# Performance work log

Hardware: AMD Instinct MI355X
Metric: run time of the kernel (lower is better)

The kernel has to match this reference:

```python
import jax, jax.numpy as jnp
import numpy as np

WIN_SIZE = 11
WIN_SIGMA = 1.5
DATA_RANGE = 255.0
K1, K2 = 0.01, 0.03


def _gauss_win():
    # matches _fspecial_gauss_1d(11, 1.5)
    coords = jnp.arange(WIN_SIZE, dtype=jnp.float32) - WIN_SIZE // 2
    g = jnp.exp(-(coords ** 2) / (2.0 * WIN_SIGMA ** 2))
    return g / g.sum()


def _gaussian_filter(x, win):
    # separable depthwise blur, 'valid' padding (padding=0 in torch), groups=C
    C = x.shape[1]
    dn = ('NCHW', 'OIHW', 'NCHW')
    kh = jnp.tile(win.reshape(1, 1, WIN_SIZE, 1), (C, 1, 1, 1))
    kw = jnp.tile(win.reshape(1, 1, 1, WIN_SIZE), (C, 1, 1, 1))
    out = jax.lax.conv_general_dilated(x, kh, (1, 1), 'VALID',
                                       dimension_numbers=dn, feature_group_count=C)
    out = jax.lax.conv_general_dilated(out, kw, (1, 1), 'VALID',
                                       dimension_numbers=dn, feature_group_count=C)
    return out


def setup_inputs() -> dict:
    key = jax.random.key(0)
    k1, k2 = jax.random.split(key)
    shape = (16, 3, 512, 512)
    X = jax.random.uniform(k1, shape, dtype=jnp.float32) * DATA_RANGE
    Y = jax.random.uniform(k2, shape, dtype=jnp.float32) * DATA_RANGE
    return {'X': X, 'Y': Y}


def reference(X, Y):
    win = _gauss_win()
    C1 = (K1 * DATA_RANGE) ** 2
    C2 = (K2 * DATA_RANGE) ** 2
    mu1 = _gaussian_filter(X, win)
    mu2 = _gaussian_filter(Y, win)
    mu1_sq = mu1 * mu1
    mu2_sq = mu2 * mu2
    mu1_mu2 = mu1 * mu2
    sigma1_sq = _gaussian_filter(X * X, win) - mu1_sq
    sigma2_sq = _gaussian_filter(Y * Y, win) - mu2_sq
    sigma12 = _gaussian_filter(X * Y, win) - mu1_mu2
    cs_map = (2.0 * sigma12 + C2) / (sigma1_sq + sigma2_sq + C2)
    ssim_map = (2.0 * mu1_mu2 + C1) / (mu1_sq + mu2_sq + C1) * cs_map
    # torch: mean over channel dim then squeeze(0) (no-op for N>1)
    ssim_map = jnp.mean(ssim_map, axis=1)  # [N, H-10, W-10]
    return 1.0 - ssim_map
```

## Files before the change

kernel.cpp:

```cpp
#include <hip/hip_runtime.h>


namespace {

constexpr int NN = 16, CC = 3, HH = 512, WW = 512;
constexpr int OH = HH - 10, OW = WW - 10;
constexpr int TW = 64, TH = 32;
constexpr int SR = 48, SC = 80;
constexpr int PIT = 80;
constexpr int HPITCH = 56;
constexpr float C1c = 6.5025f;
constexpr float C2c = 58.5225f;

typedef _Float16 half8   __attribute__((ext_vector_type(8)));
typedef _Float16 half4   __attribute__((ext_vector_type(4)));
typedef float    floatv4 __attribute__((ext_vector_type(4)));

__device__ const float WF[11] = {
    0.00102838f, 0.00759876f, 0.03600077f, 0.10936069f, 0.21300553f,
    0.26601172f,
    0.21300553f, 0.10936069f, 0.03600077f, 0.00759876f, 0.00102838f
};

__global__ __launch_bounds__(256, 3)
void ssim_kernel(const float* __restrict__ X, const float* __restrict__ Y,
                 float* __restrict__ out)
{
    __shared__ __align__(16) _Float16 s_f16[CC][2][SR * PIT];
    __shared__ __align__(16) _Float16 s_ht[TW][HPITCH];
    __shared__ _Float16 s_wtab[16];

    const int tid  = threadIdx.x;
    const int lane = tid & 63;
    const int wv   = tid >> 6;
    const int col0 = blockIdx.x * TW;
    const int row0 = blockIdx.y * TH;
    const int n    = blockIdx.z;

    if (tid < 16) s_wtab[tid] = (tid < 11) ? (_Float16)WF[tid] : (_Float16)0.f;
    __syncthreads();

    half8 bfrag;
    {
        const int bn = lane & 15, kq = (lane >> 4) * 8;
        #pragma unroll
        for (int j = 0; j < 8; ++j) {
            int kk = kq + j - bn;
            kk = (kk < 0 || kk > 10) ? 11 : kk;
            bfrag[j] = s_wtab[kk];
        }
    }

    const int arow = lane & 15;
    const int aq   = lane >> 4;
    const int crow = aq * 4;

    const int sCnt = (wv < 3) ? 4 : 3;
    int srcOff[4], ldsOff[4];
    #pragma unroll
    for (int i = 0; i < 4; ++i) {
        const int c  = (wv * 4 + i) * 64 + lane;
        const int r  = c / 20;
        const int c4 = c - r * 20;
        int gr = row0 + r;        gr = gr < HH ? gr : HH - 1;
        int gc = col0 + c4 * 4;   gc = gc <= WW - 4 ? gc : WW - 4;
        srcOff[i] = gr * WW + gc;
        ldsOff[i] = r * PIT + c4 * 4;
    }

    const size_t plane = (size_t)HH * WW;
    const float* Xn = X + (size_t)n * CC * plane;
    const float* Yn = Y + (size_t)n * CC * plane;

    float4 L[CC][2][4];
    #pragma unroll
    for (int ch = 0; ch < CC; ++ch) {
        #pragma unroll
        for (int i = 0; i < 4; ++i) {
            if (i < sCnt) {
                L[ch][0][i] = *(const float4*)(Xn + (size_t)ch * plane + srcOff[i]);
                L[ch][1][i] = *(const float4*)(Yn + (size_t)ch * plane + srcOff[i]);
            }
        }
    }

    #pragma unroll
    for (int ch = 0; ch < CC; ++ch) {
        #pragma unroll
        for (int s = 0; s < 2; ++s) {
            #pragma unroll
            for (int i = 0; i < 4; ++i) {
                if (i < sCnt) {
                    float4 v = L[ch][s][i];
                    half4 h = {(_Float16)v.x, (_Float16)v.y,
                               (_Float16)v.z, (_Float16)v.w};
                    *(half4*)&s_f16[ch][s][ldsOff[i]] = h;
                }
            }
        }
    }
    __syncthreads();

    float acc[2][4] = {{0.f,0.f,0.f,0.f},{0.f,0.f,0.f,0.f}};
    const floatv4 zf = {0.f, 0.f, 0.f, 0.f};
    const int cbase = wv * 16 + aq * 8;

    for (int ch = 0; ch < CC; ++ch) {
        half8 axf[3], ayf[3];
        #pragma unroll
        for (int rc = 0; rc < 3; ++rc) {
            const int idx = (rc * 16 + arow) * PIT + cbase;
            axf[rc] = *(const half8*)&s_f16[ch][0][idx];
            ayf[rc] = *(const half8*)&s_f16[ch][1][idx];
        }

        floatv4 vfr[5][2];
        #pragma unroll
        for (int qi = 0; qi < 5; ++qi) {
            #pragma unroll
            for (int rc = 0; rc < 3; ++rc) {
                half8 a;
                if      (qi == 0) a = axf[rc] * ayf[rc];
                else if (qi == 1) a = axf[rc] * axf[rc];
                else if (qi == 2) a = axf[rc];
                else if (qi == 3) a = ayf[rc] * ayf[rc];
                else              a = ayf[rc];
                floatv4 d = __builtin_amdgcn_mfma_f32_16x16x32_f16(
                    a, bfrag, zf, 0, 0, 0);
                half4 h = {(_Float16)d[0], (_Float16)d[1],
                           (_Float16)d[2], (_Float16)d[3]};
                *(half4*)&s_ht[wv*16 + arow][rc*16 + crow] = h;
            }
            #pragma unroll
            for (int b = 0; b < 2; ++b) {
                half8 av = *(const half8*)&s_ht[wv*16 + arow][b*16 + aq*8];
                vfr[qi][b] = __builtin_amdgcn_mfma_f32_16x16x32_f16(
                    av, bfrag, zf, 0, 0, 0);
            }
        }

        #pragma unroll
        for (int b = 0; b < 2; ++b) {
            #pragma unroll
            for (int p = 0; p < 4; ++p) {
                float m1 = vfr[2][b][p], m2 = vfr[4][b][p];
                float exx = vfr[1][b][p], eyy = vfr[3][b][p],
                      exy = vfr[0][b][p];
                float m1s = m1*m1, m2s = m2*m2, m12 = m1*m2;
                float s1 = exx - m1s, s2 = eyy - m2s, s12 = exy - m12;
                float n1 = 2.f*m12 + C1c, d1 = m1s + m2s + C1c;
                float n2 = 2.f*s12 + C2c, d2 = s1 + s2 + C2c;
                acc[b][p] = fmaf(n1 * n2, __builtin_amdgcn_rcpf(d1 * d2),
                                 acc[b][p]);
            }
        }
    }

    #pragma unroll
    for (int b = 0; b < 2; ++b) {
        const int orow = row0 + b*16 + arow;
        const int ocol = col0 + wv*16 + crow;
        if (orow < OH) {
            float r0v = 1.f - acc[b][0] * (1.f/3.f);
            float r1v = 1.f - acc[b][1] * (1.f/3.f);
            float r2v = 1.f - acc[b][2] * (1.f/3.f);
            float r3v = 1.f - acc[b][3] * (1.f/3.f);
            size_t base = ((size_t)n * OH + orow) * OW + ocol;
            if (ocol + 3 < OW) {
                *(float2*)(out + base)     = make_float2(r0v, r1v);
                *(float2*)(out + base + 2) = make_float2(r2v, r3v);
            } else {
                float rs[4] = {r0v, r1v, r2v, r3v};
                #pragma unroll
                for (int p = 0; p < 4; ++p)
                    if (ocol + p < OW) out[base + p] = rs[p];
            }
        }
    }
}

}

extern "C" void kernel_launch(void* const* d_in, const int* in_sizes, int n_in,
                              void* d_out, int out_size, void* d_ws, size_t ws_size,
                              hipStream_t stream) {
    const float* X = (const float*)d_in[0];
    const float* Y = (const float*)d_in[1];
    float* out = (float*)d_out;

    dim3 grid((OW + TW - 1) / TW,
              (OH + TH - 1) / TH,
              NN);
    ssim_kernel<<<grid, 256, 0, stream>>>(X, Y, out);
}
```

Baseline: 135.9 us.

## Pipeline per-channel global loads through double-buffered LDS instead of preloading all channels

Instead of loading all three channels of X and Y into registers and LDS up front, the kernel loads one channel at a time. It prefetches the next channel's global data into registers while the MFMA blur of the current channel runs, then writes it into an alternating half of a double-buffered LDS tile. This shrinks LDS from three channel buffers to two and cuts live registers, so global latency can overlap compute. It adds a barrier per channel and lowers launch_bounds min blocks from 3 to 2, which may reduce occupancy.

```diff
diff --git a/kernel.cpp b/kernel.cpp
--- a/kernel.cpp
+++ b/kernel.cpp
@@ -6,7 +6,7 @@
 constexpr int NN = 16, CC = 3, HH = 512, WW = 512;
 constexpr int OH = HH - 10, OW = WW - 10;
 constexpr int TW = 64, TH = 32;
-constexpr int SR = 48, SC = 80;
+constexpr int SR = 48;
 constexpr int PIT = 80;
 constexpr int HPITCH = 56;
 constexpr float C1c = 6.5025f;
@@ -22,11 +22,11 @@
     0.21300553f, 0.10936069f, 0.03600077f, 0.00759876f, 0.00102838f
 };
 
-__global__ __launch_bounds__(256, 3)
+__global__ __launch_bounds__(256, 2)
 void ssim_kernel(const float* __restrict__ X, const float* __restrict__ Y,
                  float* __restrict__ out)
 {
-    __shared__ __align__(16) _Float16 s_f16[CC][2][SR * PIT];
+    __shared__ __align__(16) _Float16 s_in[2][2][SR * PIT];
     __shared__ __align__(16) _Float16 s_ht[TW][HPITCH];
     __shared__ _Float16 s_wtab[16];
 
@@ -38,18 +38,6 @@
     const int n    = blockIdx.z;
 
     if (tid < 16) s_wtab[tid] = (tid < 11) ? (_Float16)WF[tid] : (_Float16)0.f;
-    __syncthreads();
-
-    half8 bfrag;
-    {
-        const int bn = lane & 15, kq = (lane >> 4) * 8;
-        #pragma unroll
-        for (int j = 0; j < 8; ++j) {
-            int kk = kq + j - bn;
-            kk = (kk < 0 || kk > 10) ? 11 : kk;
-            bfrag[j] = s_wtab[kk];
-        }
-    }
 
     const int arow = lane & 15;
     const int aq   = lane >> 4;
@@ -72,46 +60,63 @@
     const float* Xn = X + (size_t)n * CC * plane;
     const float* Yn = Y + (size_t)n * CC * plane;
 
-    float4 L[CC][2][4];
-    #pragma unroll
-    for (int ch = 0; ch < CC; ++ch) {
+    float4 L[2][4];
+
+    auto LOAD = [&](int ch) {
         #pragma unroll
         for (int i = 0; i < 4; ++i) {
             if (i < sCnt) {
-                L[ch][0][i] = *(const float4*)(Xn + (size_t)ch * plane + srcOff[i]);
-                L[ch][1][i] = *(const float4*)(Yn + (size_t)ch * plane + srcOff[i]);
-            }
-        }
-    }
-
-    #pragma unroll
-    for (int ch = 0; ch < CC; ++ch) {
+                L[0][i] = *(const float4*)(Xn + (size_t)ch * plane + srcOff[i]);
+                L[1][i] = *(const float4*)(Yn + (size_t)ch * plane + srcOff[i]);
+            }
+        }
+    };
+    auto WRITE = [&](int b) {
         #pragma unroll
         for (int s = 0; s < 2; ++s) {
             #pragma unroll
             for (int i = 0; i < 4; ++i) {
                 if (i < sCnt) {
-                    float4 v = L[ch][s][i];
+                    float4 v = L[s][i];
                     half4 h = {(_Float16)v.x, (_Float16)v.y,
                                (_Float16)v.z, (_Float16)v.w};
-                    *(half4*)&s_f16[ch][s][ldsOff[i]] = h;
+                    *(half4*)&s_in[b][s][ldsOff[i]] = h;
                 }
             }
         }
-    }
+    };
+
+    LOAD(0);
+    WRITE(0);
     __syncthreads();
+
+    half8 bfrag;
+    {
+        const int bn = lane & 15, kq = (lane >> 4) * 8;
+        #pragma unroll
+        for (int j = 0; j < 8; ++j) {
+            int kk = kq + j - bn;
+            kk = (kk < 0 || kk > 10) ? 11 : kk;
+            bfrag[j] = s_wtab[kk];
+        }
+    }
 
     float acc[2][4] = {{0.f,0.f,0.f,0.f},{0.f,0.f,0.f,0.f}};
     const floatv4 zf = {0.f, 0.f, 0.f, 0.f};
     const int cbase = wv * 16 + aq * 8;
 
+    #pragma unroll
     for (int ch = 0; ch < CC; ++ch) {
+        const int b = ch & 1;
+
+        if (ch + 1 < CC) LOAD(ch + 1);
+
         half8 axf[3], ayf[3];
         #pragma unroll
         for (int rc = 0; rc < 3; ++rc) {
             const int idx = (rc * 16 + arow) * PIT + cbase;
-            axf[rc] = *(const half8*)&s_f16[ch][0][idx];
-            ayf[rc] = *(const half8*)&s_f16[ch][1][idx];
+            axf[rc] = *(const half8*)&s_in[b][0][idx];
+            ayf[rc] = *(const half8*)&s_in[b][1][idx];
         }
 
         floatv4 vfr[5][2];
@@ -132,39 +137,44 @@
                 *(half4*)&s_ht[wv*16 + arow][rc*16 + crow] = h;
             }
             #pragma unroll
-            for (int b = 0; b < 2; ++b) {
-                half8 av = *(const half8*)&s_ht[wv*16 + arow][b*16 + aq*8];
-                vfr[qi][b] = __builtin_amdgcn_mfma_f32_16x16x32_f16(
+            for (int bb = 0; bb < 2; ++bb) {
+                half8 av = *(const half8*)&s_ht[wv*16 + arow][bb*16 + aq*8];
+                vfr[qi][bb] = __builtin_amdgcn_mfma_f32_16x16x32_f16(
                     av, bfrag, zf, 0, 0, 0);
             }
         }
 
         #pragma unroll
-        for (int b = 0; b < 2; ++b) {
+        for (int bb = 0; bb < 2; ++bb) {
             #pragma unroll
             for (int p = 0; p < 4; ++p) {
-                float m1 = vfr[2][b][p], m2 = vfr[4][b][p];
-                float exx = vfr[1][b][p], eyy = vfr[3][b][p],
-                      exy = vfr[0][b][p];
+                float m1 = vfr[2][bb][p], m2 = vfr[4][bb][p];
+                float exx = vfr[1][bb][p], eyy = vfr[3][bb][p],
+                      exy = vfr[0][bb][p];
                 float m1s = m1*m1, m2s = m2*m2, m12 = m1*m2;
                 float s1 = exx - m1s, s2 = eyy - m2s, s12 = exy - m12;
                 float n1 = 2.f*m12 + C1c, d1 = m1s + m2s + C1c;
                 float n2 = 2.f*s12 + C2c, d2 = s1 + s2 + C2c;
-                acc[b][p] = fmaf(n1 * n2, __builtin_amdgcn_rcpf(d1 * d2),
-                                 acc[b][p]);
-            }
+                acc[bb][p] = fmaf(n1 * n2, __builtin_amdgcn_rcpf(d1 * d2),
+                                  acc[bb][p]);
+            }
+        }
+
+        if (ch + 1 < CC) {
+            WRITE((ch + 1) & 1);
+            __syncthreads();
         }
     }
 
     #pragma unroll
-    for (int b = 0; b < 2; ++b) {
-        const int orow = row0 + b*16 + arow;
+    for (int bb = 0; bb < 2; ++bb) {
+        const int orow = row0 + bb*16 + arow;
         const int ocol = col0 + wv*16 + crow;
         if (orow < OH) {
-            float r0v = 1.f - acc[b][0] * (1.f/3.f);
-            float r1v = 1.f - acc[b][1] * (1.f/3.f);
-            float r2v = 1.f - acc[b][2] * (1.f/3.f);
-            float r3v = 1.f - acc[b][3] * (1.f/3.f);
+            float r0v = 1.f - acc[bb][0] * (1.f/3.f);
+            float r1v = 1.f - acc[bb][1] * (1.f/3.f);
+            float r2v = 1.f - acc[bb][2] * (1.f/3.f);
+            float r3v = 1.f - acc[bb][3] * (1.f/3.f);
             size_t base = ((size_t)n * OH + orow) * OW + ocol;
             if (ocol + 3 < OW) {
                 *(float2*)(out + base)     = make_float2(r0v, r1v);
```

New measurement: 131.9 us. -2.9%, faster.
